# Optimization experiments

Hardware: AMD Instinct MI355X
Metric: run time of the kernel (lower is better)

The kernel has to match this reference:

```python
import jax, jax.numpy as jnp
import numpy as np
import math

D_MODEL = 1024
FFN = 4096
NUM_HEAD = 16
HEAD_DIM = 64
BATCH = 4
SEQ = 2048
EPS = 1e-5


def _lin(k, out_dim, in_dim):
    bound = 1.0 / math.sqrt(in_dim)
    k1, k2 = jax.random.split(k)
    W = jax.random.uniform(k1, (out_dim, in_dim), jnp.float32, -bound, bound)
    b = jax.random.uniform(k2, (out_dim,), jnp.float32, -bound, bound)
    return W, b


def setup_inputs() -> dict:
    key = jax.random.key(0)
    ks = jax.random.split(key, 12)
    x = jax.random.normal(ks[0], (BATCH, SEQ, D_MODEL), jnp.float32)
    mask = jnp.zeros((SEQ, SEQ), jnp.float32)  # additive mask, broadcast over [H,B,S,S]
    Wq, bq = _lin(ks[1], D_MODEL, D_MODEL)
    Wk, bk = _lin(ks[2], D_MODEL, D_MODEL)
    Wv, bv = _lin(ks[3], D_MODEL, D_MODEL)
    Wo, bo = _lin(ks[4], D_MODEL, D_MODEL)
    gamma = jnp.ones((D_MODEL,), jnp.float32)
    beta = jnp.zeros((D_MODEL,), jnp.float32)
    W1, b1 = _lin(ks[5], FFN, D_MODEL)
    W2, b2 = _lin(ks[6], FFN // 2, FFN)
    W3, b3 = _lin(ks[7], FFN // 4, FFN // 2)
    W4, b4 = _lin(ks[8], D_MODEL, FFN // 4)
    Wl, bl = _lin(ks[9], D_MODEL, D_MODEL)
    return dict(x=x, mask=mask, Wq=Wq, bq=bq, Wk=Wk, bk=bk, Wv=Wv, bv=bv,
                Wo=Wo, bo=bo, gamma=gamma, beta=beta,
                W1=W1, b1=b1, W2=W2, b2=b2, W3=W3, b3=b3, W4=W4, b4=b4,
                Wl=Wl, bl=bl)


def _layernorm(x, gamma, beta):
    mean = jnp.mean(x, axis=-1, keepdims=True)
    var = jnp.mean((x - mean) ** 2, axis=-1, keepdims=True)
    return gamma * ((x - mean) / jnp.sqrt(var + EPS)) + beta


def _attention(x, mask, Wq, bq, Wk, bk, Wv, bv, Wo, bo):
    B, S, _ = x.shape
    def heads(W, b):
        return (x @ W.T + b).reshape(B, S, NUM_HEAD, HEAD_DIM).transpose(0, 2, 1, 3)
    q, k, v = heads(Wq, bq), heads(Wk, bk), heads(Wv, bv)  # [B,H,S,D]
    scaled = jnp.einsum('bhsd,bhtd->bhst', q, k) / math.sqrt(HEAD_DIM)
    # faithful to source: permute to [H,B,S,S], add mask, softmax, NaN->0,
    # then sum over dim=1 (which is BATCH here) -> [H,S,S]
    scaled = scaled.transpose(1, 0, 2, 3) + mask
    attn = jax.nn.softmax(scaled, axis=-1)
    attn = jnp.where(jnp.isnan(attn), 0.0, attn)
    A = jnp.sum(attn, axis=1)  # [H,S,S]
    V = jnp.einsum('hst,bhtd->bhsd', A, v)  # broadcast matmul as in torch
    V = V.transpose(0, 2, 1, 3).reshape(B, S, NUM_HEAD * HEAD_DIM)
    return V @ Wo.T + bo


def _ffn(x, W1, b1, W2, b2, W3, b3, W4, b4):
    x = jax.nn.relu(x @ W1.T + b1)
    x = jax.nn.relu(x @ W2.T + b2)
    x = jax.nn.relu(x @ W3.T + b3)
    return x @ W4.T + b4


def reference(x, mask, Wq, bq, Wk, bk, Wv, bv, Wo, bo, gamma, beta,
              W1, b1, W2, b2, W3, b3, W4, b4, Wl, bl):
    res = x
    x = _attention(x, mask, Wq, bq, Wk, bk, Wv, bv, Wo, bo)
    x = _layernorm(x + res, gamma, beta)
    res = x
    x = _ffn(x, W1, b1, W2, b2, W3, b3, W4, b4)
    x = _layernorm(res + x, gamma, beta)
    return x @ Wl.T + bl
```

## Files before the change

### kernel.cpp

```cpp
#include <hip/hip_runtime.h>
#include <stdint.h>

#define SEQL 2048
#define DM 1024
#define NH 16
#define DHD 64
#define NB 4
#define MT 8192

typedef __attribute__((ext_vector_type(8))) short bf16x8;
typedef __attribute__((ext_vector_type(4))) float f32x4;

__device__ __forceinline__ unsigned short f2bf(float f) {
  uint32_t u = __builtin_bit_cast(uint32_t, f);
  return (unsigned short)((u + 0x7FFFu + ((u >> 16) & 1u)) >> 16);
}
__device__ __forceinline__ float bf2f(unsigned short h) {
  return __builtin_bit_cast(float, (uint32_t)h << 16);
}
__device__ __forceinline__ float fexp2(float x) {
  float r;
  asm volatile("v_exp_f32 %0, %1" : "=v"(r) : "v"(x));
  return r;
}
__device__ __forceinline__ uint32_t cvtpk(float lo, float hi) {
  uint32_t r;
  asm volatile("v_cvt_pk_bf16_f32 %0, %1, %2" : "=v"(r) : "v"(lo), "v"(hi));
  return r;
}
__device__ __forceinline__ void glds16(const void* g, void* l) {
  __builtin_amdgcn_global_load_lds(
      (const __attribute__((address_space(1))) void*)g,
      (__attribute__((address_space(3))) void*)l, 16, 0, 0);
}
__device__ __forceinline__ void bar() {
  asm volatile("" ::: "memory");
  __builtin_amdgcn_s_barrier();
  asm volatile("" ::: "memory");
}
__device__ __forceinline__ void vm8() { asm volatile("s_waitcnt vmcnt(8)" ::: "memory"); }
__device__ __forceinline__ void vm4() { asm volatile("s_waitcnt vmcnt(4)" ::: "memory"); }
__device__ __forceinline__ void vm2() { asm volatile("s_waitcnt vmcnt(2)" ::: "memory"); }
__device__ __forceinline__ void vm0() { asm volatile("s_waitcnt vmcnt(0)" ::: "memory"); }

__global__ __launch_bounds__(256) void cast_f32_bf16(
    const float* __restrict__ in, unsigned short* __restrict__ out, int n8) {
  int i = blockIdx.x * 256 + threadIdx.x;
  if (i >= n8) return;
  const float4* p = (const float4*)(in + (size_t)i * 8);
  float4 a = p[0], b = p[1];
  uint32_t w0 = f2bf(a.x) | ((uint32_t)f2bf(a.y) << 16);
  uint32_t w1 = f2bf(a.z) | ((uint32_t)f2bf(a.w) << 16);
  uint32_t w2 = f2bf(b.x) | ((uint32_t)f2bf(b.y) << 16);
  uint32_t w3 = f2bf(b.z) | ((uint32_t)f2bf(b.w) << 16);
  int4 v = {(int)w0, (int)w1, (int)w2, (int)w3};
  *(int4*)(out + (size_t)i * 8) = v;
}

__global__ __launch_bounds__(256) void addb(
    const unsigned short* __restrict__ a, unsigned short* __restrict__ bio, int n8) {
  int i = blockIdx.x * 256 + threadIdx.x;
  if (i >= n8) return;
  int4 va = *(const int4*)(a + (size_t)i * 8);
  int4 vb = *(const int4*)(bio + (size_t)i * 8);
  uint32_t* pa = (uint32_t*)&va;
  uint32_t* pb = (uint32_t*)&vb;
  int4 vo;
  uint32_t* po = (uint32_t*)&vo;
#pragma unroll
  for (int j = 0; j < 4; j++) {
    float lo = bf2f((unsigned short)pa[j]) + bf2f((unsigned short)pb[j]);
    float hi = bf2f((unsigned short)(pa[j] >> 16)) + bf2f((unsigned short)(pb[j] >> 16));
    po[j] = f2bf(lo) | ((uint32_t)f2bf(hi) << 16);
  }
  *(int4*)(bio + (size_t)i * 8) = vo;
}

__global__ __launch_bounds__(256) void vtrans(
    const unsigned short* __restrict__ V, unsigned short* __restrict__ Vt) {
  __shared__ unsigned short td[64][72];
  const int blk = blockIdx.x;
  const int t64 = blk & 31;
  const int b = (blk >> 5) & 3;
  const int h = blk >> 7;
  const int tid = threadIdx.x;
  const int r = tid >> 3, c8 = (tid & 7) * 8;
  const unsigned short* src = V + (size_t)(b * SEQL + t64 * 64) * DM + h * 64;
#pragma unroll
  for (int half = 0; half < 2; half++) {
    int4 v = *(const int4*)(src + (size_t)(r + half * 32) * DM + c8);
    *(int4*)&td[r + half * 32][c8] = v;
  }
  __syncthreads();
  unsigned short* dst = Vt + (size_t)((h * 4 + b) * 64) * SEQL + t64 * 64;
#pragma unroll
  for (int half = 0; half < 2; half++) {
    int tk = tid + half * 256;
    int d = tk >> 3, tc = (tk & 7) * 8;
    int gq = (tc >> 3) & 3;
    int b32 = tc & 32;
    unsigned short tmp[8];
#pragma unroll
    for (int j = 0; j < 8; j++)
      tmp[j] = td[b32 + gq * 4 + (j & 3) + 16 * (j >> 2)][d];
    *(int4*)(dst + (size_t)d * SEQL + tc) = *(int4*)tmp;
  }
}

template <int MS, int NS, int MR, int MH>
__device__ __forceinline__ void mmaQ(f32x4 (&acc)[MR][4],
                                     const bf16x8 (&Ar)[MH][2],
                                     const bf16x8 (&Br)[2][2]) {
  __builtin_amdgcn_s_setprio(1);
#pragma unroll
  for (int m = 0; m < MH; m++)
#pragma unroll
    for (int n = 0; n < 2; n++)
#pragma unroll
      for (int kk = 0; kk < 2; kk++)
        acc[MS * MH + m][NS * 2 + n] = __builtin_amdgcn_mfma_f32_16x16x32_bf16(
            Ar[m][kk], Br[n][kk], acc[MS * MH + m][NS * 2 + n], 0, 0, 0);
  __builtin_amdgcn_s_setprio(0);
}

template <int MH>
__device__ __forceinline__ void loadF(bf16x8 (&Ar)[MH][2], const char* base,
                                      int row0, int g) {
#pragma unroll
  for (int m = 0; m < MH; m++) {
    int row = row0 + m * 16;
    int sw = (row & 7) << 4;
    Ar[m][0] = *(const bf16x8*)(base + row * 128 + ((g << 4) ^ sw));
    Ar[m][1] = *(const bf16x8*)(base + row * 128 + (((4 + g) << 4) ^ sw));
  }
}

template <int BM, bool RELU, int OMODE>
__global__ __launch_bounds__(512, 1) void gemm8(
    const unsigned short* __restrict__ Ag, const unsigned short* __restrict__ Bg,
    const float* __restrict__ bias0, const float* __restrict__ bias1,
    const float* __restrict__ bias2, void* C0, void* C1, void* C2, int N, int K,
    float sc0) {
  constexpr int MR = BM / 32;
  constexpr int MH = MR / 2;
  constexpr int AT = BM * 128;
  constexpr int BT = 256 * 128;
  __shared__ __align__(16) char lds[2 * AT + 2 * BT];
  char* Ab0 = lds;
  char* Ab1 = lds + AT;
  char* Bb0 = lds + 2 * AT;
  char* Bb1 = lds + 2 * AT + BT;

  const int tid = threadIdx.x;
  const int wid = tid >> 6, lane = tid & 63;
  const int wr = wid >> 2, wc = wid & 3;
  const int g = lane >> 4, ln = lane & 15;

  const int nbx = N >> 8;
  const int nwg = gridDim.x;
  const int cpx = nwg >> 3;
  const int wg = (blockIdx.x & 7) * cpx + (blockIdx.x >> 3);
  const int bm = wg / nbx, bn = wg % nbx;

  f32x4 acc[MR][4];
#pragma unroll
  for (int m = 0; m < MR; m++)
#pragma unroll
    for (int n = 0; n < 4; n++) acc[m][n] = (f32x4){0.f, 0.f, 0.f, 0.f};

  const int srow = wid * 8 + (lane >> 3);
  const int cs8 = ((lane & 7) ^ (lane >> 3)) * 8;
  const unsigned short* aBase = Ag + (size_t)(bm * BM + srow) * K + cs8;
  const unsigned short* bBase = Bg + (size_t)(bn * 256 + srow) * K + cs8;
  const int wofs = wid * 1024;

  auto stageA = [&](char* buf, int tt, int h) {
    const unsigned short* src = aBase + (size_t)(h * (BM / 2)) * K + tt * 64;
    char* dst = buf + h * (AT / 2) + wofs;
    glds16(src, dst);
    if constexpr (BM == 256) glds16(src + (size_t)64 * K, dst + 8192);
  };
  auto stageB = [&](char* buf, int tt, int h) {
    const unsigned short* src = bBase + (size_t)(h * 128) * K + tt * 64;
    char* dst = buf + h * (BT / 2) + wofs;
    glds16(src, dst);
    glds16(src + (size_t)64 * K, dst + 8192);
  };

  const int np = K >> 7;
  const int rowA0 = wr * (BM / 2) + ln;
  const int rowB0 = wc * 64 + ln;

  stageA(Ab0, 0, 0);
  stageA(Ab0, 0, 1);
  stageB(Bb0, 0, 0);
  stageB(Bb0, 0, 1);
  stageB(Bb1, 1, 0);
  stageB(Bb1, 1, 1);
  vm4();
  bar();

  bf16x8 Ar0[MH][2], Ar1[MH][2], Br0[2][2], Br1[2][2];
  for (int i = 0; i < np; i++) {
    const int t = 2 * i;
    const bool sg = (i + 1 < np);
    loadF<MH>(Ar0, Ab0, rowA0, g);
    loadF<2>(Br0, Bb0, rowB0, g);
    loadF<2>(Br1, Bb0, rowB0 + 32, g);
    stageA(Ab1, t + 1, 0);
    bar();
    mmaQ<0, 0>(acc, Ar0, Br0);
    bar();
    loadF<MH>(Ar1, Ab0, rowA0 + MH * 16, g);
    stageA(Ab1, t + 1, 1);
    bar();
    mmaQ<0, 1>(acc, Ar0, Br1);
    bar();
    if (sg) stageB(Bb0, t + 2, 0);
    bar();
    mmaQ<1, 1>(acc, Ar1, Br1);
    bar();
    if (sg) stageB(Bb0, t + 2, 1);
    bar();
    mmaQ<1, 0>(acc, Ar1, Br0);
    if (sg) vm4(); else vm0();
    bar();
    loadF<MH>(Ar0, Ab1, rowA0, g);
    loadF<2>(Br0, Bb1, rowB0, g);
    loadF<2>(Br1, Bb1, rowB0 + 32, g);
    if (sg) stageA(Ab0, t + 2, 0);
    bar();
    mmaQ<0, 0>(acc, Ar0, Br0);
    bar();
    loadF<MH>(Ar1, Ab1, rowA0 + MH * 16, g);
    if (sg) stageA(Ab0, t + 2, 1);
    bar();
    mmaQ<0, 1>(acc, Ar0, Br1);
    bar();
    if (sg) stageB(Bb1, t + 3, 0);
    bar();
    mmaQ<1, 1>(acc, Ar1, Br1);
    bar();
    if (sg) stageB(Bb1, t + 3, 1);
    bar();
    mmaQ<1, 0>(acc, Ar1, Br0);
    if (sg) vm4();
    bar();
  }

  const int c0 = bn * 256 + wc * 64;
  const float* bias = bias0;
  float scl = sc0;
  unsigned short* outb = (unsigned short*)C0;
  float* outf = (float*)C0;
  int ldC = N;
  if constexpr (OMODE == 2) {
    int seg = bn >> 2;
    bias = seg == 0 ? bias0 : (seg == 1 ? bias1 : bias2);
    outb = (unsigned short*)(seg == 0 ? C0 : (seg == 1 ? C1 : C2));
    scl = seg == 0 ? sc0 : 1.0f;
    ldC = 1024;
  }
#pragma unroll
  for (int am = 0; am < MR; am++) {
#pragma unroll
    for (int n = 0; n < 4; n++) {
      int col = c0 + n * 16 + ln;
      int colL = (OMODE == 2) ? (col & 1023) : col;
      float bv = bias[colL];
#pragma unroll
      for (int r = 0; r < 4; r++) {
        int row = bm * BM + wr * (BM / 2) + am * 16 + g * 4 + r;
        float v = (acc[am][n][r] + bv) * scl;
        if constexpr (RELU) v = fmaxf(v, 0.f);
        if constexpr (OMODE == 0)
          outf[(size_t)row * ldC + colL] = v;
        else
          outb[(size_t)row * ldC + colL] = f2bf(v);
      }
    }
  }
}

__global__ __launch_bounds__(256, 4) void attn_stats(
    const unsigned short* __restrict__ Q, const unsigned short* __restrict__ Kb,
    float* __restrict__ lst) {
  __shared__ unsigned short sK[2][64 * 64];
  const int blk = (blockIdx.x & 7) * 128 + (blockIdx.x >> 3);
  const int sblk = blk & 15;
  const int bh = blk >> 4;
  const int b = bh >> 4, h = bh & 15;
  const int tid = threadIdx.x;
  const int wid = tid >> 6, lane = tid & 63;
  const int g = lane >> 4, ln = lane & 15;
  const int s0 = sblk * 128 + wid * 32;

  bf16x8 q[2][2];
#pragma unroll
  for (int s = 0; s < 2; s++) {
    const unsigned short* qp =
        Q + (size_t)(b * SEQL + s0 + s * 16 + ln) * DM + h * DHD + g * 8;
    q[s][0] = *(const bf16x8*)qp;
    q[s][1] = *(const bf16x8*)(qp + 32);
  }

  const int srow = tid >> 3;
  const int sch = (tid & 7) ^ (srow & 7);
  const unsigned short* kg =
      Kb + (size_t)(b * SEQL + srow) * DM + h * DHD + sch * 8;

  auto stage = [&](int buf, int t0) {
    glds16(kg + (size_t)t0 * DM, (char*)&sK[buf][0] + wid * 1024);
    glds16(kg + (size_t)(t0 + 32) * DM, (char*)&sK[buf][0] + 4096 + wid * 1024);
  };

  float lsum[2] = {0.f, 0.f};
  const int NT = SEQL / 64;
  stage(0, 0);
  vm0();
  bar();
  int cur = 0;
  for (int i = 0; i < NT; i++) {
    if (i + 1 < NT) {
      stage(cur ^ 1, (i + 1) * 64);
      vm2();
    } else {
      vm0();
    }
    bar();
#pragma unroll
    for (int tt = 0; tt < 4; tt++) {
      int row = tt * 16 + ln;
      const char* base = (const char*)&sK[cur][0] + row * 128;
      bf16x8 k0 = *(const bf16x8*)(base + ((g ^ (row & 7)) << 4));
      bf16x8 k1 = *(const bf16x8*)(base + (((4 + g) ^ (row & 7)) << 4));
      f32x4 sa = {0.f, 0.f, 0.f, 0.f}, sb = {0.f, 0.f, 0.f, 0.f};
      sa = __builtin_amdgcn_mfma_f32_16x16x32_bf16(k0, q[0][0], sa, 0, 0, 0);
      sa = __builtin_amdgcn_mfma_f32_16x16x32_bf16(k1, q[0][1], sa, 0, 0, 0);
      sb = __builtin_amdgcn_mfma_f32_16x16x32_bf16(k0, q[1][0], sb, 0, 0, 0);
      sb = __builtin_amdgcn_mfma_f32_16x16x32_bf16(k1, q[1][1], sb, 0, 0, 0);
      lsum[0] += fexp2(sa[0]) + fexp2(sa[1]) + fexp2(sa[2]) + fexp2(sa[3]);
      lsum[1] += fexp2(sb[0]) + fexp2(sb[1]) + fexp2(sb[2]) + fexp2(sb[3]);
    }
    bar();
    cur ^= 1;
  }
#pragma unroll
  for (int s = 0; s < 2; s++) {
    lsum[s] += __shfl_xor(lsum[s], 16);
    lsum[s] += __shfl_xor(lsum[s], 32);
    if (lane < 16) lst[(size_t)bh * SEQL + s0 + s * 16 + lane] = lsum[s];
  }
}

__global__ __launch_bounds__(256, 2) void attn_apply(
    const unsigned short* __restrict__ Q, const unsigned short* __restrict__ Kb,
    const unsigned short* __restrict__ Vtp, const float* __restrict__ lst,
    unsigned short* __restrict__ op0, unsigned short* __restrict__ op1) {
  __shared__ unsigned short sK[2][4][32 * 64];
  __shared__ unsigned short sV[2][4][64 * 32];
  const int blk = (blockIdx.x & 7) * 64 + (blockIdx.x >> 3);
  const int tpart = blk & 1;
  const int sblk = (blk >> 1) & 15;
  const int h = blk >> 5;
  const int tid = threadIdx.x;
  const int wid = tid >> 6, lane = tid & 63;
  const int g = lane >> 4, ln = lane & 15;
  const int s0 = sblk * 128 + wid * 32;
  const int tbase = tpart * (SEQL / 2);

  bf16x8 q[2][4][2];
#pragma unroll
  for (int s = 0; s < 2; s++)
#pragma unroll
    for (int b = 0; b < 4; b++) {
      const unsigned short* qp =
          Q + (size_t)(b * SEQL + s0 + s * 16 + ln) * DM + h * DHD + g * 8;
      q[s][b][0] = *(const bf16x8*)qp;
      q[s][b][1] = *(const bf16x8*)(qp + 32);
    }
  float rl[2][4];
#pragma unroll
  for (int s = 0; s < 2; s++)
#pragma unroll
    for (int b = 0; b < 4; b++)
      rl[s][b] = 1.0f / lst[(size_t)(b * NH + h) * SEQL + s0 + s * 16 + ln];

  f32x4 o[2][4][4];
#pragma unroll
  for (int s = 0; s < 2; s++)
#pragma unroll
    for (int b = 0; b < 4; b++)
#pragma unroll
      for (int c = 0; c < 4; c++) o[s][b][c] = (f32x4){0.f, 0.f, 0.f, 0.f};

  const int krow = tid >> 3;
  const int kch = (tid & 7) ^ (krow & 7);
  const int vrow = wid * 16 + (lane >> 2);
  const int vch = (lane & 3) ^ ((vrow >> 1) & 3);
  const unsigned short* vbase = Vtp + (size_t)(h * 256 + vrow) * SEQL + vch * 8;
  const int vswz = (ln >> 1) & 3;

  auto stage = [&](int buf, int t0) {
#pragma unroll
    for (int b = 0; b < 4; b++)
      glds16(Kb + (size_t)(b * SEQL + t0 + krow) * DM + h * DHD + kch * 8,
             (char*)&sK[buf][b][0] + wid * 1024);
#pragma unroll
    for (int b = 0; b < 4; b++)
      glds16(vbase + (size_t)(b * 64) * SEQL + t0,
             (char*)&sV[buf][b][0] + wid * 1024);
  };

  const int NT = (SEQL / 2) / 32;
  stage(0, tbase);
  vm0();
  bar();
  int cur = 0;
  for (int i = 0; i < NT; i++) {
    if (i + 1 < NT) {
      stage(cur ^ 1, tbase + (i + 1) * 32);
      vm8();
    } else {
      vm0();
    }
    bar();

    float at0[2][4], at1[2][4];
#pragma unroll
    for (int tt = 0; tt < 2; tt++)
#pragma unroll
      for (int r = 0; r < 4; r++) { at0[tt][r] = 0.f; at1[tt][r] = 0.f; }
#pragma unroll
    for (int b = 0; b < 4; b++) {
#pragma unroll
      for (int tt = 0; tt < 2; tt++) {
        int row = tt * 16 + ln;
        const char* base = (const char*)&sK[cur][b][0] + row * 128;
        bf16x8 k0 = *(const bf16x8*)(base + ((g ^ (row & 7)) << 4));
        bf16x8 k1 = *(const bf16x8*)(base + (((4 + g) ^ (row & 7)) << 4));
        f32x4 sa = {0.f, 0.f, 0.f, 0.f}, sb = {0.f, 0.f, 0.f, 0.f};
        sa = __builtin_amdgcn_mfma_f32_16x16x32_bf16(k0, q[0][b][0], sa, 0, 0, 0);
        sa = __builtin_amdgcn_mfma_f32_16x16x32_bf16(k1, q[0][b][1], sa, 0, 0, 0);
        sb = __builtin_amdgcn_mfma_f32_16x16x32_bf16(k0, q[1][b][0], sb, 0, 0, 0);
        sb = __builtin_amdgcn_mfma_f32_16x16x32_bf16(k1, q[1][b][1], sb, 0, 0, 0);
#pragma unroll
        for (int r = 0; r < 4; r++) {
          at0[tt][r] = fmaf(fexp2(sa[r]), rl[0][b], at0[tt][r]);
          at1[tt][r] = fmaf(fexp2(sb[r]), rl[1][b], at1[tt][r]);
        }
      }
    }
    int4 aw0 = {(int)cvtpk(at0[0][0], at0[0][1]), (int)cvtpk(at0[0][2], at0[0][3]),
                (int)cvtpk(at0[1][0], at0[1][1]), (int)cvtpk(at0[1][2], at0[1][3])};
    int4 aw1 = {(int)cvtpk(at1[0][0], at1[0][1]), (int)cvtpk(at1[0][2], at1[0][3]),
                (int)cvtpk(at1[1][0], at1[1][1]), (int)cvtpk(at1[1][2], at1[1][3])};
    bf16x8 apk0 = __builtin_bit_cast(bf16x8, aw0);
    bf16x8 apk1 = __builtin_bit_cast(bf16x8, aw1);

#pragma unroll
    for (int b = 0; b < 4; b++) {
#pragma unroll
      for (int c = 0; c < 4; c++) {
        int row = c * 16 + ln;
        const char* vb =
            (const char*)&sV[cur][b][0] + row * 64 + ((g ^ vswz) << 4);
        bf16x8 vf = *(const bf16x8*)vb;
        o[0][b][c] = __builtin_amdgcn_mfma_f32_16x16x32_bf16(apk0, vf, o[0][b][c], 0, 0, 0);
        o[1][b][c] = __builtin_amdgcn_mfma_f32_16x16x32_bf16(apk1, vf, o[1][b][c], 0, 0, 0);
      }
    }
    bar();
    cur ^= 1;
  }

  unsigned short* op = tpart ? op1 : op0;
#pragma unroll
  for (int s = 0; s < 2; s++)
#pragma unroll
    for (int b = 0; b < 4; b++)
#pragma unroll
      for (int c = 0; c < 4; c++)
#pragma unroll
        for (int r = 0; r < 4; r++) {
          int srow = s0 + s * 16 + g * 4 + r;
          size_t off = (size_t)(b * SEQL + srow) * DM + h * DHD + c * 16 + ln;
          op[off] = f2bf(o[s][b][c][r]);
        }
}

template <bool RESBF16>
__global__ __launch_bounds__(256) void ln_kernel(
    const float* __restrict__ a, const void* __restrict__ res,
    const float* __restrict__ gamma, const float* __restrict__ beta,
    unsigned short* __restrict__ obf) {
  __shared__ float red[8];
  const int row = blockIdx.x;
  const int tid = threadIdx.x;
  const size_t base = (size_t)row * DM + tid * 4;
  float4 va = *(const float4*)(a + base);
  float v0, v1, v2, v3;
  if (RESBF16) {
    const unsigned short* rp = (const unsigned short*)res + base;
    ushort4 u = *(const ushort4*)rp;
    v0 = va.x + bf2f(u.x);
    v1 = va.y + bf2f(u.y);
    v2 = va.z + bf2f(u.z);
    v3 = va.w + bf2f(u.w);
  } else {
    float4 vr = *(const float4*)((const float*)res + base);
    v0 = va.x + vr.x;
    v1 = va.y + vr.y;
    v2 = va.z + vr.z;
    v3 = va.w + vr.w;
  }
  float sum = v0 + v1 + v2 + v3;
#pragma unroll
  for (int off = 1; off < 64; off <<= 1) sum += __shfl_xor(sum, off);
  const int wid = tid >> 6, lane = tid & 63;
  if (lane == 0) red[wid] = sum;
  __syncthreads();
  float mean = (red[0] + red[1] + red[2] + red[3]) * (1.0f / DM);
  float d0 = v0 - mean, d1 = v1 - mean, d2 = v2 - mean, d3 = v3 - mean;
  float sq = d0 * d0 + d1 * d1 + d2 * d2 + d3 * d3;
#pragma unroll
  for (int off = 1; off < 64; off <<= 1) sq += __shfl_xor(sq, off);
  if (lane == 0) red[4 + wid] = sq;
  __syncthreads();
  float var = (red[4] + red[5] + red[6] + red[7]) * (1.0f / DM);
  float rstd = rsqrtf(var + 1e-5f);
  float4 gm = *(const float4*)(gamma + tid * 4);
  float4 bb = *(const float4*)(beta + tid * 4);
  float o0 = gm.x * (d0 * rstd) + bb.x;
  float o1 = gm.y * (d1 * rstd) + bb.y;
  float o2 = gm.z * (d2 * rstd) + bb.z;
  float o3 = gm.w * (d3 * rstd) + bb.w;
  uint32_t w0 = f2bf(o0) | ((uint32_t)f2bf(o1) << 16);
  uint32_t w1 = f2bf(o2) | ((uint32_t)f2bf(o3) << 16);
  uint2 pk = {w0, w1};
  *(uint2*)(obf + base) = pk;
}

extern "C" void kernel_launch(void* const* d_in, const int* in_sizes, int n_in,
                              void* d_out, int out_size, void* d_ws, size_t ws_size,
                              hipStream_t stream) {
  (void)in_sizes; (void)n_in; (void)out_size; (void)ws_size;
  const float* x  = (const float*)d_in[0];
  const float* Wq = (const float*)d_in[2];  const float* bq = (const float*)d_in[3];
  const float* Wk = (const float*)d_in[4];  const float* bk = (const float*)d_in[5];
  const float* Wv = (const float*)d_in[6];  const float* bv = (const float*)d_in[7];
  const float* Wo = (const float*)d_in[8];  const float* bo = (const float*)d_in[9];
  const float* gamma = (const float*)d_in[10]; const float* beta = (const float*)d_in[11];
  const float* W1 = (const float*)d_in[12]; const float* b1 = (const float*)d_in[13];
  const float* W2 = (const float*)d_in[14]; const float* b2 = (const float*)d_in[15];
  const float* W3 = (const float*)d_in[16]; const float* b3 = (const float*)d_in[17];
  const float* W4 = (const float*)d_in[18]; const float* b4 = (const float*)d_in[19];
  const float* Wl = (const float*)d_in[20]; const float* bl = (const float*)d_in[21];
  float* out = (float*)d_out;

  char* w = (char*)d_ws;
  const size_t MB = 1024 * 1024;
  unsigned short* xb   = (unsigned short*)(w);
  unsigned short* Qb   = (unsigned short*)(w + 16 * MB);
  unsigned short* Kbf  = (unsigned short*)(w + 32 * MB);
  unsigned short* Vbf  = (unsigned short*)(w + 48 * MB);
  float* lst = (float*)(w + 64 * MB);
  unsigned short* ctx  = (unsigned short*)(w + 65 * MB);
  unsigned short* wbuf = (unsigned short*)(w + 81 * MB);
  float* aproj = (float*)(w + 97 * MB);
  unsigned short* ln1b = (unsigned short*)(w + 129 * MB);
  unsigned short* Vt   = (unsigned short*)(w + 97 * MB);
  unsigned short* op0  = (unsigned short*)(w);
  unsigned short* h1   = (unsigned short*)(w);
  unsigned short* h2   = (unsigned short*)(w + 97 * MB);
  unsigned short* h3   = (unsigned short*)(w + 65 * MB);
  float* ffo  = (float*)(w);
  unsigned short* ln2b = (unsigned short*)(w + 32 * MB);

  auto cast = [&](const float* src, unsigned short* dst, size_t n) {
    int n8 = (int)(n / 8);
    cast_f32_bf16<<<dim3((n8 + 255) / 256), dim3(256), 0, stream>>>(src, dst, n8);
  };
  const float QSCALE = 0.125f * 1.44269504088896f;

  cast(x, xb, (size_t)MT * DM);
  cast(Wq, wbuf, (size_t)DM * DM);
  cast(Wk, wbuf + (size_t)DM * DM, (size_t)DM * DM);
  cast(Wv, wbuf + (size_t)2 * DM * DM, (size_t)DM * DM);
  gemm8<256, false, 2><<<dim3((MT / 256) * (3072 / 256)), dim3(512), 0, stream>>>(
      xb, wbuf, bq, bk, bv, Qb, Kbf, Vbf, 3072, 1024, QSCALE);
  vtrans<<<dim3(NH * NB * (SEQL / 64)), dim3(256), 0, stream>>>(Vbf, Vt);
  attn_stats<<<dim3(NB * NH * 16), dim3(256), 0, stream>>>(Qb, Kbf, lst);
  attn_apply<<<dim3(NH * 16 * 2), dim3(256), 0, stream>>>(Qb, Kbf, Vt, lst, op0, ctx);
  addb<<<dim3((MT * DM / 8 + 255) / 256), dim3(256), 0, stream>>>(op0, ctx, MT * DM / 8);
  cast(Wo, wbuf, (size_t)DM * DM);
  gemm8<128, false, 0><<<dim3((MT / 128) * 4), dim3(512), 0, stream>>>(
      ctx, wbuf, bo, nullptr, nullptr, aproj, nullptr, nullptr, 1024, 1024, 1.0f);
  ln_kernel<false><<<dim3(MT), dim3(256), 0, stream>>>(aproj, x, gamma, beta, ln1b);
  cast(W1, wbuf, (size_t)4096 * DM);
  gemm8<256, true, 1><<<dim3((MT / 256) * 16), dim3(512), 0, stream>>>(
      ln1b, wbuf, b1, nullptr, nullptr, h1, nullptr, nullptr, 4096, 1024, 1.0f);
  cast(W2, wbuf, (size_t)2048 * 4096);
  gemm8<256, true, 1><<<dim3((MT / 256) * 8), dim3(512), 0, stream>>>(
      h1, wbuf, b2, nullptr, nullptr, h2, nullptr, nullptr, 2048, 4096, 1.0f);
  cast(W3, wbuf, (size_t)1024 * 2048);
  gemm8<128, true, 1><<<dim3((MT / 128) * 4), dim3(512), 0, stream>>>(
      h2, wbuf, b3, nullptr, nullptr, h3, nullptr, nullptr, 1024, 2048, 1.0f);
  cast(W4, wbuf, (size_t)DM * DM);
  gemm8<128, false, 0><<<dim3((MT / 128) * 4), dim3(512), 0, stream>>>(
      h3, wbuf, b4, nullptr, nullptr, ffo, nullptr, nullptr, 1024, 1024, 1.0f);
  ln_kernel<true><<<dim3(MT), dim3(256), 0, stream>>>(ffo, ln1b, gamma, beta, ln2b);
  cast(Wl, wbuf, (size_t)DM * DM);
  gemm8<128, false, 0><<<dim3((MT / 128) * 4), dim3(512), 0, stream>>>(
      ln2b, wbuf, bl, nullptr, nullptr, out, nullptr, nullptr, 1024, 1024, 1.0f);
}
```

Before: 647.1 us.

## Use 32x32x16 MFMA tiles for the 256-row GEMMs and raise occupancy hint

Adds a gemm8w kernel for the 256x256-tile GEMMs (QKV, FFN1, FFN2) that uses mfma_f32_32x32x16_bf16 with f32x16 accumulators instead of 16x16x32 tiles. Fragment loads and the epilogue row/column mapping are rewritten for the 32-lane layout. The intent is fewer LDS fragment reads per FLOP and better MFMA throughput. The 128-row gemm8 is specialised to BM=128, and both kernels' launch bounds change from 1 to 2 waves-per-EU minimum, which may force register spilling with the large accumulator arrays.

```diff
diff --git a/kernel.cpp b/kernel.cpp
--- a/kernel.cpp
+++ b/kernel.cpp
@@ -10,6 +10,7 @@
 
 typedef __attribute__((ext_vector_type(8))) short bf16x8;
 typedef __attribute__((ext_vector_type(4))) float f32x4;
+typedef __attribute__((ext_vector_type(16))) float f32x16;
 
 __device__ __forceinline__ unsigned short f2bf(float f) {
   uint32_t u = __builtin_bit_cast(uint32_t, f);
@@ -107,43 +108,45 @@
   }
 }
 
-template <int MS, int NS, int MR, int MH>
-__device__ __forceinline__ void mmaQ(f32x4 (&acc)[MR][4],
-                                     const bf16x8 (&Ar)[MH][2],
-                                     const bf16x8 (&Br)[2][2]) {
+template <int MS, int NS>
+__device__ __forceinline__ void mmaW(f32x16 (&acc)[4][2],
+                                     const bf16x8 (&Ar)[2][4],
+                                     const bf16x8 (&Bn)[4]) {
   __builtin_amdgcn_s_setprio(1);
 #pragma unroll
-  for (int m = 0; m < MH; m++)
-#pragma unroll
-    for (int n = 0; n < 2; n++)
-#pragma unroll
-      for (int kk = 0; kk < 2; kk++)
-        acc[MS * MH + m][NS * 2 + n] = __builtin_amdgcn_mfma_f32_16x16x32_bf16(
-            Ar[m][kk], Br[n][kk], acc[MS * MH + m][NS * 2 + n], 0, 0, 0);
+  for (int kk = 0; kk < 4; kk++)
+#pragma unroll
+    for (int mt = 0; mt < 2; mt++)
+      acc[MS * 2 + mt][NS] = __builtin_amdgcn_mfma_f32_32x32x16_bf16(
+          Ar[mt][kk], Bn[kk], acc[MS * 2 + mt][NS], 0, 0, 0);
   __builtin_amdgcn_s_setprio(0);
 }
-
-template <int MH>
-__device__ __forceinline__ void loadF(bf16x8 (&Ar)[MH][2], const char* base,
-                                      int row0, int g) {
-#pragma unroll
-  for (int m = 0; m < MH; m++) {
-    int row = row0 + m * 16;
+__device__ __forceinline__ void loadA32(bf16x8 (&Ar)[2][4], const char* base,
+                                        int row0, int gh) {
+#pragma unroll
+  for (int mt = 0; mt < 2; mt++) {
+    int row = row0 + mt * 32;
     int sw = (row & 7) << 4;
-    Ar[m][0] = *(const bf16x8*)(base + row * 128 + ((g << 4) ^ sw));
-    Ar[m][1] = *(const bf16x8*)(base + row * 128 + (((4 + g) << 4) ^ sw));
-  }
-}
-
-template <int BM, bool RELU, int OMODE>
-__global__ __launch_bounds__(512, 1) void gemm8(
+#pragma unroll
+    for (int kk = 0; kk < 4; kk++)
+      Ar[mt][kk] = *(const bf16x8*)(base + row * 128 + (((kk * 2 + gh) << 4) ^ sw));
+  }
+}
+__device__ __forceinline__ void loadB32(bf16x8 (&Bn)[4], const char* base,
+                                        int row, int gh) {
+  int sw = (row & 7) << 4;
+#pragma unroll
+  for (int kk = 0; kk < 4; kk++)
+    Bn[kk] = *(const bf16x8*)(base + row * 128 + (((kk * 2 + gh) << 4) ^ sw));
+}
+
+template <bool RELU, int OMODE>
+__global__ __launch_bounds__(512, 2) void gemm8w(
     const unsigned short* __restrict__ Ag, const unsigned short* __restrict__ Bg,
     const float* __restrict__ bias0, const float* __restrict__ bias1,
     const float* __restrict__ bias2, void* C0, void* C1, void* C2, int N, int K,
     float sc0) {
-  constexpr int MR = BM / 32;
-  constexpr int MH = MR / 2;
-  constexpr int AT = BM * 128;
+  constexpr int AT = 256 * 128;
   constexpr int BT = 256 * 128;
   __shared__ __align__(16) char lds[2 * AT + 2 * BT];
   char* Ab0 = lds;
@@ -154,7 +157,7 @@
   const int tid = threadIdx.x;
   const int wid = tid >> 6, lane = tid & 63;
   const int wr = wid >> 2, wc = wid & 3;
-  const int g = lane >> 4, ln = lane & 15;
+  const int gh = lane >> 5, l32 = lane & 31;
 
   const int nbx = N >> 8;
   const int nwg = gridDim.x;
@@ -162,23 +165,25 @@
   const int wg = (blockIdx.x & 7) * cpx + (blockIdx.x >> 3);
   const int bm = wg / nbx, bn = wg % nbx;
 
-  f32x4 acc[MR][4];
-#pragma unroll
-  for (int m = 0; m < MR; m++)
-#pragma unroll
-    for (int n = 0; n < 4; n++) acc[m][n] = (f32x4){0.f, 0.f, 0.f, 0.f};
+  f32x16 acc[4][2];
+#pragma unroll
+  for (int m = 0; m < 4; m++)
+#pragma unroll
+    for (int n = 0; n < 2; n++)
+#pragma unroll
+      for (int e = 0; e < 16; e++) acc[m][n][e] = 0.f;
 
   const int srow = wid * 8 + (lane >> 3);
   const int cs8 = ((lane & 7) ^ (lane >> 3)) * 8;
-  const unsigned short* aBase = Ag + (size_t)(bm * BM + srow) * K + cs8;
+  const unsigned short* aBase = Ag + (size_t)(bm * 256 + srow) * K + cs8;
   const unsigned short* bBase = Bg + (size_t)(bn * 256 + srow) * K + cs8;
   const int wofs = wid * 1024;
 
   auto stageA = [&](char* buf, int tt, int h) {
-    const unsigned short* src = aBase + (size_t)(h * (BM / 2)) * K + tt * 64;
+    const unsigned short* src = aBase + (size_t)(h * 128) * K + tt * 64;
     char* dst = buf + h * (AT / 2) + wofs;
     glds16(src, dst);
-    if constexpr (BM == 256) glds16(src + (size_t)64 * K, dst + 8192);
+    glds16(src + (size_t)64 * K, dst + 8192);
   };
   auto stageB = [&](char* buf, int tt, int h) {
     const unsigned short* src = bBase + (size_t)(h * 128) * K + tt * 64;
@@ -188,8 +193,8 @@
   };
 
   const int np = K >> 7;
-  const int rowA0 = wr * (BM / 2) + ln;
-  const int rowB0 = wc * 64 + ln;
+  const int rowA0 = wr * 128 + l32;
+  const int rowB0 = wc * 64 + l32;
 
   stageA(Ab0, 0, 0);
   stageA(Ab0, 0, 1);
@@ -200,50 +205,50 @@
   vm4();
   bar();
 
-  bf16x8 Ar0[MH][2], Ar1[MH][2], Br0[2][2], Br1[2][2];
+  bf16x8 Ar0[2][4], Ar1[2][4], Bn0[4], Bn1[4];
   for (int i = 0; i < np; i++) {
     const int t = 2 * i;
     const bool sg = (i + 1 < np);
-    loadF<MH>(Ar0, Ab0, rowA0, g);
-    loadF<2>(Br0, Bb0, rowB0, g);
-    loadF<2>(Br1, Bb0, rowB0 + 32, g);
+    loadA32(Ar0, Ab0, rowA0, gh);
+    loadB32(Bn0, Bb0, rowB0, gh);
     stageA(Ab1, t + 1, 0);
     bar();
-    mmaQ<0, 0>(acc, Ar0, Br0);
-    bar();
-    loadF<MH>(Ar1, Ab0, rowA0 + MH * 16, g);
+    mmaW<0, 0>(acc, Ar0, Bn0);
+    bar();
+    loadB32(Bn1, Bb0, rowB0 + 32, gh);
     stageA(Ab1, t + 1, 1);
     bar();
-    mmaQ<0, 1>(acc, Ar0, Br1);
-    bar();
+    mmaW<0, 1>(acc, Ar0, Bn1);
+    bar();
+    loadA32(Ar1, Ab0, rowA0 + 64, gh);
     if (sg) stageB(Bb0, t + 2, 0);
     bar();
-    mmaQ<1, 1>(acc, Ar1, Br1);
+    mmaW<1, 1>(acc, Ar1, Bn1);
     bar();
     if (sg) stageB(Bb0, t + 2, 1);
     bar();
-    mmaQ<1, 0>(acc, Ar1, Br0);
+    mmaW<1, 0>(acc, Ar1, Bn0);
     if (sg) vm4(); else vm0();
     bar();
-    loadF<MH>(Ar0, Ab1, rowA0, g);
-    loadF<2>(Br0, Bb1, rowB0, g);
-    loadF<2>(Br1, Bb1, rowB0 + 32, g);
+    loadA32(Ar0, Ab1, rowA0, gh);
+    loadB32(Bn0, Bb1, rowB0, gh);
     if (sg) stageA(Ab0, t + 2, 0);
     bar();
-    mmaQ<0, 0>(acc, Ar0, Br0);
-    bar();
-    loadF<MH>(Ar1, Ab1, rowA0 + MH * 16, g);
+    mmaW<0, 0>(acc, Ar0, Bn0);
+    bar();
+    loadB32(Bn1, Bb1, rowB0 + 32, gh);
     if (sg) stageA(Ab0, t + 2, 1);
     bar();
-    mmaQ<0, 1>(acc, Ar0, Br1);
-    bar();
+    mmaW<0, 1>(acc, Ar0, Bn1);
+    bar();
+    loadA32(Ar1, Ab1, rowA0 + 64, gh);
     if (sg) stageB(Bb1, t + 3, 0);
     bar();
-    mmaQ<1, 1>(acc, Ar1, Br1);
+    mmaW<1, 1>(acc, Ar1, Bn1);
     bar();
     if (sg) stageB(Bb1, t + 3, 1);
     bar();
-    mmaQ<1, 0>(acc, Ar1, Br0);
+    mmaW<1, 0>(acc, Ar1, Bn0);
     if (sg) vm4();
     bar();
   }
@@ -262,21 +267,189 @@
     ldC = 1024;
   }
 #pragma unroll
+  for (int mt = 0; mt < 4; mt++) {
+#pragma unroll
+    for (int nt = 0; nt < 2; nt++) {
+      int col = c0 + nt * 32 + l32;
+      int colL = (OMODE == 2) ? (col & 1023) : col;
+      float bv = bias[colL];
+      int rb = bm * 256 + wr * 128 + mt * 32 + 4 * gh;
+#pragma unroll
+      for (int rg = 0; rg < 16; rg++) {
+        int row = rb + (rg & 3) + 8 * (rg >> 2);
+        float v = (acc[mt][nt][rg] + bv) * scl;
+        if constexpr (RELU) v = fmaxf(v, 0.f);
+        if constexpr (OMODE == 0)
+          outf[(size_t)row * ldC + colL] = v;
+        else
+          outb[(size_t)row * ldC + colL] = f2bf(v);
+      }
+    }
+  }
+}
+
+template <int MS, int NS, int MR, int MH>
+__device__ __forceinline__ void mmaQ(f32x4 (&acc)[MR][4],
+                                     const bf16x8 (&Ar)[MH][2],
+                                     const bf16x8 (&Br)[2][2]) {
+  __builtin_amdgcn_s_setprio(1);
+#pragma unroll
+  for (int m = 0; m < MH; m++)
+#pragma unroll
+    for (int n = 0; n < 2; n++)
+#pragma unroll
+      for (int kk = 0; kk < 2; kk++)
+        acc[MS * MH + m][NS * 2 + n] = __builtin_amdgcn_mfma_f32_16x16x32_bf16(
+            Ar[m][kk], Br[n][kk], acc[MS * MH + m][NS * 2 + n], 0, 0, 0);
+  __builtin_amdgcn_s_setprio(0);
+}
+
+template <int MH>
+__device__ __forceinline__ void loadF(bf16x8 (&Ar)[MH][2], const char* base,
+                                      int row0, int g) {
+#pragma unroll
+  for (int m = 0; m < MH; m++) {
+    int row = row0 + m * 16;
+    int sw = (row & 7) << 4;
+    Ar[m][0] = *(const bf16x8*)(base + row * 128 + ((g << 4) ^ sw));
+    Ar[m][1] = *(const bf16x8*)(base + row * 128 + (((4 + g) << 4) ^ sw));
+  }
+}
+
+template <bool RELU, int OMODE>
+__global__ __launch_bounds__(512, 2) void gemm8(
+    const unsigned short* __restrict__ Ag, const unsigned short* __restrict__ Bg,
+    const float* __restrict__ bias0, const float* __restrict__ bias1,
+    const float* __restrict__ bias2, void* C0, void* C1, void* C2, int N, int K,
+    float sc0) {
+  constexpr int BM = 128;
+  constexpr int MR = BM / 32;
+  constexpr int MH = MR / 2;
+  constexpr int AT = BM * 128;
+  constexpr int BT = 256 * 128;
+  __shared__ __align__(16) char lds[2 * AT + 2 * BT];
+  char* Ab0 = lds;
+  char* Ab1 = lds + AT;
+  char* Bb0 = lds + 2 * AT;
+  char* Bb1 = lds + 2 * AT + BT;
+
+  const int tid = threadIdx.x;
+  const int wid = tid >> 6, lane = tid & 63;
+  const int wr = wid >> 2, wc = wid & 3;
+  const int g = lane >> 4, ln = lane & 15;
+
+  const int nbx = N >> 8;
+  const int nwg = gridDim.x;
+  const int cpx = nwg >> 3;
+  const int wg = (blockIdx.x & 7) * cpx + (blockIdx.x >> 3);
+  const int bm = wg / nbx, bn = wg % nbx;
+
+  f32x4 acc[MR][4];
+#pragma unroll
+  for (int m = 0; m < MR; m++)
+#pragma unroll
+    for (int n = 0; n < 4; n++) acc[m][n] = (f32x4){0.f, 0.f, 0.f, 0.f};
+
+  const int srow = wid * 8 + (lane >> 3);
+  const int cs8 = ((lane & 7) ^ (lane >> 3)) * 8;
+  const unsigned short* aBase = Ag + (size_t)(bm * BM + srow) * K + cs8;
+  const unsigned short* bBase = Bg + (size_t)(bn * 256 + srow) * K + cs8;
+  const int wofs = wid * 1024;
+
+  auto stageA = [&](char* buf, int tt, int h) {
+    const unsigned short* src = aBase + (size_t)(h * (BM / 2)) * K + tt * 64;
+    char* dst = buf + h * (AT / 2) + wofs;
+    glds16(src, dst);
+  };
+  auto stageB = [&](char* buf, int tt, int h) {
+    const unsigned short* src = bBase + (size_t)(h * 128) * K + tt * 64;
+    char* dst = buf + h * (BT / 2) + wofs;
+    glds16(src, dst);
+    glds16(src + (size_t)64 * K, dst + 8192);
+  };
+
+  const int np = K >> 7;
+  const int rowA0 = wr * (BM / 2) + ln;
+  const int rowB0 = wc * 64 + ln;
+
+  stageA(Ab0, 0, 0);
+  stageA(Ab0, 0, 1);
+  stageB(Bb0, 0, 0);
+  stageB(Bb0, 0, 1);
+  stageB(Bb1, 1, 0);
+  stageB(Bb1, 1, 1);
+  vm4();
+  bar();
+
+  bf16x8 Ar0[MH][2], Ar1[MH][2], Br0[2][2], Br1[2][2];
+  for (int i = 0; i < np; i++) {
+    const int t = 2 * i;
+    const bool sg = (i + 1 < np);
+    loadF<MH>(Ar0, Ab0, rowA0, g);
+    loadF<2>(Br0, Bb0, rowB0, g);
+    loadF<2>(Br1, Bb0, rowB0 + 32, g);
+    stageA(Ab1, t + 1, 0);
+    bar();
+    mmaQ<0, 0>(acc, Ar0, Br0);
+    bar();
+    loadF<MH>(Ar1, Ab0, rowA0 + MH * 16, g);
+    stageA(Ab1, t + 1, 1);
+    bar();
+    mmaQ<0, 1>(acc, Ar0, Br1);
+    bar();
+    if (sg) stageB(Bb0, t + 2, 0);
+    bar();
+    mmaQ<1, 1>(acc, Ar1, Br1);
+    bar();
+    if (sg) stageB(Bb0, t + 2, 1);
+    bar();
+    mmaQ<1, 0>(acc, Ar1, Br0);
+    if (sg) vm4(); else vm0();
+    bar();
+    loadF<MH>(Ar0, Ab1, rowA0, g);
+    loadF<2>(Br0, Bb1, rowB0, g);
+    loadF<2>(Br1, Bb1, rowB0 + 32, g);
+    if (sg) stageA(Ab0, t + 2, 0);
+    bar();
+    mmaQ<0, 0>(acc, Ar0, Br0);
+    bar();
+    loadF<MH>(Ar1, Ab1, rowA0 + MH * 16, g);
+    if (sg) stageA(Ab0, t + 2, 1);
+    bar();
+    mmaQ<0, 1>(acc, Ar0, Br1);
+    bar();
+    if (sg) stageB(Bb1, t + 3, 0);
+    bar();
+    mmaQ<1, 1>(acc, Ar1, Br1);
+    bar();
+    if (sg) stageB(Bb1, t + 3, 1);
+    bar();
+    mmaQ<1, 0>(acc, Ar1, Br0);
+    if (sg) vm4();
+    bar();
+  }
+
+  const int c0 = bn * 256 + wc * 64;
+  const float* bias = bias0;
+  float scl = sc0;
+  unsigned short* outb = (unsigned short*)C0;
+  float* outf = (float*)C0;
+  int ldC = N;
+#pragma unroll
   for (int am = 0; am < MR; am++) {
 #pragma unroll
     for (int n = 0; n < 4; n++) {
       int col = c0 + n * 16 + ln;
-      int colL = (OMODE == 2) ? (col & 1023) : col;
-      float bv = bias[colL];
+      float bv = bias[col];
 #pragma unroll
       for (int r = 0; r < 4; r++) {
         int row = bm * BM + wr * (BM / 2) + am * 16 + g * 4 + r;
         float v = (acc[am][n][r] + bv) * scl;
         if constexpr (RELU) v = fmaxf(v, 0.f);
         if constexpr (OMODE == 0)
-          outf[(size_t)row * ldC + colL] = v;
+          outf[(size_t)row * ldC + col] = v;
         else
-          outb[(size_t)row * ldC + colL] = f2bf(v);
+          outb[(size_t)row * ldC + col] = f2bf(v);
       }
     }
   }
@@ -587,30 +760,30 @@
   cast(Wq, wbuf, (size_t)DM * DM);
   cast(Wk, wbuf + (size_t)DM * DM, (size_t)DM * DM);
   cast(Wv, wbuf + (size_t)2 * DM * DM, (size_t)DM * DM);
-  gemm8<256, false, 2><<<dim3((MT / 256) * (3072 / 256)), dim3(512), 0, stream>>>(
+  gemm8w<false, 2><<<dim3((MT / 256) * (3072 / 256)), dim3(512), 0, stream>>>(
       xb, wbuf, bq, bk, bv, Qb, Kbf, Vbf, 3072, 1024, QSCALE);
   vtrans<<<dim3(NH * NB * (SEQL / 64)), dim3(256), 0, stream>>>(Vbf, Vt);
   attn_stats<<<dim3(NB * NH * 16), dim3(256), 0, stream>>>(Qb, Kbf, lst);
   attn_apply<<<dim3(NH * 16 * 2), dim3(256), 0, stream>>>(Qb, Kbf, Vt, lst, op0, ctx);
   addb<<<dim3((MT * DM / 8 + 255) / 256), dim3(256), 0, stream>>>(op0, ctx, MT * DM / 8);
   cast(Wo, wbuf, (size_t)DM * DM);
-  gemm8<128, false, 0><<<dim3((MT / 128) * 4), dim3(512), 0, stream>>>(
+  gemm8<false, 0><<<dim3((MT / 128) * 4), dim3(512), 0, stream>>>(
       ctx, wbuf, bo, nullptr, nullptr, aproj, nullptr, nullptr, 1024, 1024, 1.0f);
   ln_kernel<false><<<dim3(MT), dim3(256), 0, stream>>>(aproj, x, gamma, beta, ln1b);
   cast(W1, wbuf, (size_t)4096 * DM);
-  gemm8<256, true, 1><<<dim3((MT / 256) * 16), dim3(512), 0, stream>>>(
+  gemm8w<true, 1><<<dim3((MT / 256) * 16), dim3(512), 0, stream>>>(
       ln1b, wbuf, b1, nullptr, nullptr, h1, nullptr, nullptr, 4096, 1024, 1.0f);
   cast(W2, wbuf, (size_t)2048 * 4096);
-  gemm8<256, true, 1><<<dim3((MT / 256) * 8), dim3(512), 0, stream>>>(
+  gemm8w<true, 1><<<dim3((MT / 256) * 8), dim3(512), 0, stream>>>(
       h1, wbuf, b2, nullptr, nullptr, h2, nullptr, nullptr, 2048, 4096, 1.0f);
   cast(W3, wbuf, (size_t)1024 * 2048);
-  gemm8<128, true, 1><<<dim3((MT / 128) * 4), dim3(512), 0, stream>>>(
+  gemm8<true, 1><<<dim3((MT / 128) * 4), dim3(512), 0, stream>>>(
       h2, wbuf, b3, nullptr, nullptr, h3, nullptr, nullptr, 1024, 2048, 1.0f);
   cast(W4, wbuf, (size_t)DM * DM);
-  gemm8<128, false, 0><<<dim3((MT / 128) * 4), dim3(512), 0, stream>>>(
+  gemm8<false, 0><<<dim3((MT / 128) * 4), dim3(512), 0, stream>>>(
       h3, wbuf, b4, nullptr, nullptr, ffo, nullptr, nullptr, 1024, 1024, 1.0f);
   ln_kernel<true><<<dim3(MT), dim3(256), 0, stream>>>(ffo, ln1b, gamma, beta, ln2b);
   cast(Wl, wbuf, (size_t)DM * DM);
-  gemm8<128, false, 0><<<dim3((MT / 128) * 4), dim3(512), 0, stream>>>(
+  gemm8<false, 0><<<dim3((MT / 128) * 4), dim3(512), 0, stream>>>(
       ln2b, wbuf, bl, nullptr, nullptr, out, nullptr, nullptr, 1024, 1024, 1.0f);
 }
```

Result: faster. 608.1 us (-6.0%).
